# Kernel optimization log

Hardware: AMD Instinct MI355X
Metric: run time of the kernel (lower is better)

Reference implementation:

```python
import jax, jax.numpy as jnp
import numpy as np

SDIM, VDIM, HID, DEPTH = 128, 3, 64, 4
N, E = 50000, 800000
CUTOFF = 5.0


def setup_inputs() -> dict:
    key = jax.random.key(0)
    ks = jax.random.split(key, 16)
    s = jax.random.normal(ks[0], (N, SDIM), jnp.float32)
    v = jax.random.normal(ks[1], (N, 3, VDIM), jnp.float32)
    edge_index = jax.random.randint(ks[2], (2, E), 0, N, dtype=jnp.int32).astype(jnp.int64)
    d = jax.random.uniform(ks[3], (E,), jnp.float32) * CUTOFF
    r = jax.random.normal(ks[4], (E, 3), jnp.float32)
    r = r / jnp.linalg.norm(r, axis=-1, keepdims=True)
    batch = jnp.zeros((N,), jnp.int64)

    def w(k, shape):
        return jax.random.normal(k, shape, jnp.float32) / jnp.sqrt(jnp.float32(shape[-2]))

    return {
        's': s, 'v': v, 'edge_index': edge_index, 'd': d, 'r': r, 'batch': batch,
        'We1': w(ks[5], (DEPTH, 2 * SDIM + 1, HID)), 'be1': jnp.zeros((DEPTH, HID), jnp.float32),
        'We2': w(ks[6], (DEPTH, HID, HID)), 'be2': jnp.zeros((DEPTH, HID), jnp.float32),
        'Wn1': w(ks[7], (DEPTH, SDIM + HID, HID)), 'bn1': jnp.zeros((DEPTH, HID), jnp.float32),
        'Wn2': w(ks[8], (DEPTH, HID, SDIM)), 'bn2': jnp.zeros((DEPTH, SDIM), jnp.float32),
        'Wv': w(ks[9], (DEPTH, HID, 2 * VDIM)), 'bv': jnp.zeros((DEPTH, 2 * VDIM), jnp.float32),
    }


def _egcl(s, v, src, dst, d, r, C, deg, We1, be1, We2, be2, Wn1, bn1, Wn2, bn2, Wv, bv):
    n = s.shape[0]
    # edge message MLP on gathered endpoint features + distance
    x = jnp.concatenate([s[dst], s[src], d[:, None]], axis=-1)   # [E, 2*SDIM+1]
    h = jax.nn.silu(x @ We1 + be1)
    h = jax.nn.silu(h @ We2 + be2)
    h = h * C[:, None]                                            # cutoff envelope
    # scalar update
    agg_s = jax.ops.segment_sum(h, dst, num_segments=n)           # [N, HID]
    u = jax.nn.silu(jnp.concatenate([s, agg_s], axis=-1) @ Wn1 + bn1)
    s = s + (u @ Wn2 + bn2)
    # equivariant vector update: gated neighbor vectors + gated edge directions
    gates = h @ Wv + bv                                           # [E, 2*VDIM]
    g1, g2 = gates[:, :VDIM], gates[:, VDIM:]
    mv = v[src] * g1[:, None, :] + r[:, :, None] * g2[:, None, :] # [E, 3, VDIM]
    agg_v = jax.ops.segment_sum(mv, dst, num_segments=n) / deg[:, None, None]  # mean aggr
    v = v + agg_v
    return s, v


def reference(s, v, edge_index, d, r, batch, We1, be1, We2, be2, Wn1, bn1, Wn2, bn2, Wv, bv):
    src, dst = edge_index[0], edge_index[1]
    C = 0.5 * (jnp.cos(jnp.pi * d / CUTOFF) + 1.0) * (d < CUTOFF).astype(d.dtype)
    deg = jax.ops.segment_sum(jnp.ones_like(d), dst, num_segments=s.shape[0])
    deg = jnp.maximum(deg, 1.0)
    for i in range(DEPTH):
        s, v = _egcl(s, v, src, dst, d, r, C, deg,
                     We1[i], be1[i], We2[i], be2[i],
                     Wn1[i], bn1[i], Wn2[i], bn2[i], Wv[i], bv[i])
    return (s, v)
```

## Files before the change

### kernel.cpp

```cpp
#include <hip/hip_runtime.h>
#include <math.h>

#define SDIM 128
#define HID 64
#define DEPTH 4
#define CUTOFF_F 5.0f
#define CHUNK 4096

typedef __attribute__((ext_vector_type(8))) short bf16x8;
typedef __attribute__((ext_vector_type(4))) float f32x4;
typedef float4 __attribute__((aligned(4))) float4_u;

__device__ __forceinline__ float silu_f(float x) {
    float e = __expf(-x);
    return x * __builtin_amdgcn_rcpf(1.0f + e);
}

__device__ __forceinline__ unsigned short f2bf(float x) {
    __bf16 b = (__bf16)x;
    return __builtin_bit_cast(unsigned short, b);
}
__device__ __forceinline__ unsigned int f2bf2(float a, float b) {
    return (unsigned int)f2bf(a) | ((unsigned int)f2bf(b) << 16);
}
__device__ __forceinline__ float bf2f(unsigned short u) {
    return __uint_as_float(((unsigned int)u) << 16);
}

struct f8 { float v[8]; };
__device__ __forceinline__ f8 load8(const float* p) {
    f8 r;
    float4 a = *(const float4*)p;
    float4 b = *(const float4*)(p + 4);
    r.v[0]=a.x; r.v[1]=a.y; r.v[2]=a.z; r.v[3]=a.w;
    r.v[4]=b.x; r.v[5]=b.y; r.v[6]=b.z; r.v[7]=b.w;
    return r;
}
__device__ __forceinline__ bf16x8 pack8(const float* h) {
    bf16x8 o;
#pragma unroll
    for (int j = 0; j < 8; ++j) o[j] = (short)f2bf(h[j]);
    return o;
}
__device__ __forceinline__ void unpack8(bf16x8 b, float* o) {
#pragma unroll
    for (int j = 0; j < 8; ++j)
        o[j] = __uint_as_float(((unsigned int)(unsigned short)b[j]) << 16);
}

__global__ void detect_idx_kernel(const void* ei, int N, int* flag) {
    int lane = threadIdx.x;
    const long long* p64 = (const long long*)ei;
    long long v = p64[lane];
    bool ok = (v >= 0 && v < (long long)N);
    unsigned long long m = __ballot(ok);
    if (lane == 0) *flag = (m == ~0ull) ? 1 : 0;
}

__global__ void decode_idx_kernel(const void* ei, int E, int N, const int* flag,
                                  int* __restrict__ srcw, int* __restrict__ dstw,
                                  int* __restrict__ deg_i) {
    int i = blockIdx.x * blockDim.x + threadIdx.x;
    if (i >= 2 * E) return;
    int v;
    if (*flag) v = (int)((const long long*)ei)[i];
    else       v = ((const int*)ei)[i];
    v = min(max(v, 0), N - 1);
    if (i < E) {
        srcw[i] = v;
    } else {
        dstw[i - E] = v;
        atomicAdd(&deg_i[v], 1);
    }
}

__global__ __launch_bounds__(256) void scan1_kernel(const int* __restrict__ deg_i,
                                                    int* __restrict__ part, int N) {
    __shared__ int wsum[4];
    int b = blockIdx.x, t = threadIdx.x;
    int base = b * CHUNK;
    int sum = 0;
    for (int i = t; i < CHUNK; i += 256) {
        int idx = base + i;
        sum += (idx < N) ? deg_i[idx] : 0;
    }
#pragma unroll
    for (int off = 32; off; off >>= 1) sum += __shfl_down(sum, off, 64);
    if ((t & 63) == 0) wsum[t >> 6] = sum;
    __syncthreads();
    if (t == 0) part[b] = wsum[0] + wsum[1] + wsum[2] + wsum[3];
}

__global__ void scan2_kernel(int* __restrict__ part, int* __restrict__ row_start,
                             int B1, int N) {
    int t = threadIdx.x;
    int v = (t < B1) ? part[t] : 0;
    int incl = v;
#pragma unroll
    for (int off = 1; off < 64; off <<= 1) {
        int x = __shfl_up(incl, off, 64);
        if (t >= off) incl += x;
    }
    if (t < B1) part[t] = incl - v;
    if (t == 63) row_start[N] = incl;
}

__global__ __launch_bounds__(256) void scan3_kernel(const int* __restrict__ deg_i,
                                                    const int* __restrict__ part,
                                                    int* __restrict__ row_start, int N) {
    __shared__ int wsum[4];
    __shared__ int carry_s;
    int b = blockIdx.x, t = threadIdx.x;
    int lane = t & 63, w = t >> 6;
    if (t == 0) carry_s = part[b];
    __syncthreads();
    int base0 = b * CHUNK;
    for (int base = base0; base < base0 + CHUNK; base += 256) {
        int i = base + t;
        int v = (i < N) ? deg_i[i] : 0;
        int incl = v;
#pragma unroll
        for (int off = 1; off < 64; off <<= 1) {
            int x = __shfl_up(incl, off, 64);
            if (lane >= off) incl += x;
        }
        if (lane == 63) wsum[w] = incl;
        __syncthreads();
        int wpre = 0;
#pragma unroll
        for (int k = 0; k < 4; ++k) if (k < w) wpre += wsum[k];
        int total = wsum[0] + wsum[1] + wsum[2] + wsum[3];
        int carry = carry_s;
        if (i < N) row_start[i] = carry + wpre + incl - v;
        __syncthreads();
        if (t == 0) carry_s = carry + total;
        __syncthreads();
    }
}

__global__ void scatter_kernel(const int* __restrict__ srcw, const int* __restrict__ dstw,
                               const float* __restrict__ dvec, const float* __restrict__ rvec,
                               const int* __restrict__ row_start, int* __restrict__ cursor,
                               float* __restrict__ rec, int E) {
    int e = blockIdx.x * blockDim.x + threadIdx.x;
    if (e >= E) return;
    int dd = dstw[e];
    int ofs = atomicAdd(&cursor[dd], 1);
    int pos = row_start[dd] + ofs;
    float dv = dvec[e];
    float c = 0.5f * (cosf(3.14159265358979323846f * dv * (1.0f / CUTOFF_F)) + 1.0f);
    c = (dv < CUTOFF_F) ? c : 0.0f;
    float4 r0 = make_float4(__int_as_float(srcw[e]), __int_as_float(dd), dv, c);
    float4 r1 = make_float4(rvec[(size_t)e * 3 + 0], rvec[(size_t)e * 3 + 1],
                            rvec[(size_t)e * 3 + 2], 0.0f);
    *(float4*)(rec + (size_t)pos * 8)     = r0;
    *(float4*)(rec + (size_t)pos * 8 + 4) = r1;
}

__global__ __launch_bounds__(256) void wprep_kernel(
    const float* __restrict__ We1, const float* __restrict__ We2,
    const float* __restrict__ Wv,  const float* __restrict__ Wn1,
    const float* __restrict__ Wn2,
    unsigned short* __restrict__ We1t, unsigned short* __restrict__ We2t,
    unsigned short* __restrict__ Wvt,  unsigned short* __restrict__ Wn1t,
    unsigned short* __restrict__ Wn2t) {
    int l = blockIdx.x, t = threadIdx.x;
    const float* W2 = We2 + (size_t)l * HID * HID;
    unsigned short* T2 = We2t + (size_t)l * HID * HID;
    for (int idx = t; idx < HID * HID; idx += 256) {
        int n = idx >> 6, k = idx & 63;
        T2[n * 64 + k] = f2bf(W2[k * HID + n]);
    }
    const float* Wvl = Wv + (size_t)l * HID * 6;
    unsigned short* Tv = Wvt + (size_t)l * 16 * 64;
    for (int idx = t; idx < 16 * 64; idx += 256) {
        int n = idx >> 6, k = idx & 63;
        Tv[idx] = (n < 6) ? f2bf(Wvl[k * 6 + n]) : (unsigned short)0;
    }
    const float* W1 = We1 + (size_t)l * 257 * 64;
    unsigned short* T1 = We1t + (size_t)l * 128 * 128;
    for (int idx = t; idx < 128 * 128; idx += 256) {
        int n = idx >> 7, k = idx & 127;
        float w = (n < 64) ? W1[(size_t)k * 64 + n] : W1[(size_t)(k + 128) * 64 + (n - 64)];
        T1[n * 128 + k] = f2bf(w);
    }
    const float* Wn1l = Wn1 + (size_t)l * 192 * 64;
    unsigned short* Tn1 = Wn1t + (size_t)l * 64 * 192;
    for (int idx = t; idx < 64 * 192; idx += 256) {
        int n = idx / 192, k = idx - n * 192;
        Tn1[idx] = f2bf(Wn1l[(size_t)k * 64 + n]);
    }
    const float* Wn2l = Wn2 + (size_t)l * 64 * 128;
    unsigned short* Tn2 = Wn2t + (size_t)l * 128 * 64;
    for (int idx = t; idx < 128 * 64; idx += 256) {
        int n = idx >> 6, k = idx & 63;
        Tn2[idx] = f2bf(Wn2l[(size_t)k * 128 + n]);
    }
}

__global__ __launch_bounds__(64) void node_pre_kernel(
    const float* __restrict__ s, const unsigned short* __restrict__ We1t,
    const float* __restrict__ be1,
    unsigned short* __restrict__ Pa, unsigned short* __restrict__ Pb, int N)
{
    __shared__ unsigned short sa[16 * 136];
    int lane = threadIdx.x;
    int n0 = blockIdx.x * 16;
    for (int idx = lane; idx < 512; idx += 64) {
        int rl = idx >> 5, c4 = (idx & 31) << 2;
        int n = n0 + rl;
        float4 val = make_float4(0.f, 0.f, 0.f, 0.f);
        if (n < N) val = *(const float4*)(s + (size_t)n * SDIM + c4);
        *(uint2*)(sa + rl * 136 + c4) = make_uint2(f2bf2(val.x, val.y), f2bf2(val.z, val.w));
    }
    __builtin_amdgcn_wave_barrier();
    int lm = lane & 15, lq = lane >> 4;
    int nr = n0 + lm;
    bool rowok = (nr < N);

    bf16x8 af[4];
#pragma unroll
    for (int kc = 0; kc < 4; ++kc)
        af[kc] = *(const bf16x8*)(sa + lm * 136 + kc * 32 + lq * 8);

#pragma unroll
    for (int ct = 0; ct < 8; ++ct) {
        f32x4 acc = {0.f, 0.f, 0.f, 0.f};
#pragma unroll
        for (int kc = 0; kc < 4; ++kc) {
            bf16x8 b = *(const bf16x8*)(We1t + (size_t)(ct * 16 + lm) * 128 + kc * 32 + lq * 8);
            acc = __builtin_amdgcn_mfma_f32_16x16x32_bf16(b, af[kc], acc, 0, 0, 0);
        }
        if (rowok) {
            if (ct < 4) {
                float4 b4 = *(const float4*)(be1 + ct * 16 + lq * 4);
                *(uint2*)(Pa + (size_t)nr * HID + ct * 16 + lq * 4) =
                    make_uint2(f2bf2(acc[0] + b4.x, acc[1] + b4.y),
                               f2bf2(acc[2] + b4.z, acc[3] + b4.w));
            } else {
                *(uint2*)(Pb + (size_t)nr * HID + (ct - 4) * 16 + lq * 4) =
                    make_uint2(f2bf2(acc[0], acc[1]), f2bf2(acc[2], acc[3]));
            }
        }
    }
}

__global__ __launch_bounds__(256) void edge_kernel(
    const float* __restrict__ rec,
    const unsigned short* __restrict__ Pa, const unsigned short* __restrict__ Pb,
    const float* __restrict__ wd,
    const unsigned short* __restrict__ We2t, const float* __restrict__ be2,
    const unsigned short* __restrict__ Wvt, const float* __restrict__ bv,
    const float* __restrict__ v,
    float* __restrict__ agg_s, float* __restrict__ agg_v, int E)
{
    __shared__ unsigned short hb[64 * 72];
    __shared__ float  gl[64 * 8];
    __shared__ float  vb[64 * 12];
    __shared__ int    m_dst[64];
    __shared__ float4 m_r4[64];
    int t = threadIdx.x;
    int e0 = blockIdx.x * 64;
    int lane = t & 63, w = t >> 6;
    int lm = lane & 15, lq = lane >> 4;
    int m0 = w * 16, rm = m0 + lm;
    int ka = lq * 8, kb = 32 + lq * 8;

    int e  = e0 + rm;
    int ec = min(e, E - 1);
    float4 r0 = *(const float4*)(rec + (size_t)ec * 8);
    int srcr = __float_as_int(r0.x);
    int dstr = __float_as_int(r0.y);
    float dv = r0.z;
    float Cr = (e < E) ? r0.w : 0.0f;

    const unsigned short* pa = Pa + (size_t)dstr * HID;
    const unsigned short* pb = Pb + (size_t)srcr * HID;
    bf16x8 ba0 = *(const bf16x8*)(pa + ka);
    bf16x8 bb0 = *(const bf16x8*)(pb + ka);
    bf16x8 ba1 = *(const bf16x8*)(pa + kb);
    bf16x8 bb1 = *(const bf16x8*)(pb + kb);
    f8 xw = load8(wd + ka), yw = load8(wd + kb);

    if (lq == 0) {
        m_dst[rm] = dstr;
        m_r4[rm]  = *(const float4*)(rec + (size_t)ec * 8 + 4);
    }
    {
        const float* vr = v + (size_t)srcr * 9;
        if (lq < 2) {
            float4_u a = *(const float4_u*)(vr + lq * 4);
            *(float4*)(vb + rm * 12 + lq * 4) = make_float4(a.x, a.y, a.z, a.w);
        } else if (lq == 2) {
            vb[rm * 12 + 8] = vr[8];
        }
    }
    bf16x8 wv0 = *(const bf16x8*)(Wvt + (size_t)lm * 64 + ka);
    bf16x8 wv1 = *(const bf16x8*)(Wvt + (size_t)lm * 64 + kb);

    bf16x8 afr0, afr1;
    {
        float fa[8], fb[8], h1[8];
        unpack8(ba0, fa); unpack8(bb0, fb);
#pragma unroll
        for (int j = 0; j < 8; ++j) h1[j] = silu_f(fa[j] + fb[j] + dv * xw.v[j]);
        afr0 = pack8(h1);
        unpack8(ba1, fa); unpack8(bb1, fb);
#pragma unroll
        for (int j = 0; j < 8; ++j) h1[j] = silu_f(fa[j] + fb[j] + dv * yw.v[j]);
        afr1 = pack8(h1);
    }

#pragma unroll
    for (int t4 = 0; t4 < 4; ++t4) {
        bf16x8 a0 = *(const bf16x8*)(We2t + (size_t)(t4 * 16 + lm) * 64 + ka);
        bf16x8 a1 = *(const bf16x8*)(We2t + (size_t)(t4 * 16 + lm) * 64 + kb);
        f32x4 a = {0.f, 0.f, 0.f, 0.f};
        a = __builtin_amdgcn_mfma_f32_16x16x32_bf16(a0, afr0, a, 0, 0, 0);
        a = __builtin_amdgcn_mfma_f32_16x16x32_bf16(a1, afr1, a, 0, 0, 0);
        float4 b4 = *(const float4*)(be2 + t4 * 16 + lq * 4);
        unsigned int p0 = f2bf2(silu_f(a[0] + b4.x) * Cr, silu_f(a[1] + b4.y) * Cr);
        unsigned int p1 = f2bf2(silu_f(a[2] + b4.z) * Cr, silu_f(a[3] + b4.w) * Cr);
        *(uint2*)(hb + rm * 72 + t4 * 16 + lq * 4) = make_uint2(p0, p1);
    }
    __builtin_amdgcn_wave_barrier();

    {
        bf16x8 hb0 = *(const bf16x8*)(hb + rm * 72 + ka);
        bf16x8 hb1 = *(const bf16x8*)(hb + rm * 72 + kb);
        f32x4 ga = {0.f, 0.f, 0.f, 0.f};
        ga = __builtin_amdgcn_mfma_f32_16x16x32_bf16(wv0, hb0, ga, 0, 0, 0);
        ga = __builtin_amdgcn_mfma_f32_16x16x32_bf16(wv1, hb1, ga, 0, 0, 0);
        int er2 = m0 + lm;
        if (lq == 0) {
            float4_u bb = *(const float4_u*)bv;
            *(float4*)(gl + er2 * 8) =
                make_float4(ga[0] + bb.x, ga[1] + bb.y, ga[2] + bb.z, ga[3] + bb.w);
        } else if (lq == 1) {
            gl[er2 * 8 + 4] = ga[0] + bv[4];
            gl[er2 * 8 + 5] = ga[1] + bv[5];
        }
    }

    {
        int c = lane;
        float acc = 0.f;
        int cur = m_dst[m0];
#pragma unroll 4
        for (int r = m0; r < m0 + 16; ++r) {
            int dr = m_dst[r];
            if (dr != cur) {
                atomicAdd(&agg_s[(size_t)cur * HID + c], acc);
                acc = 0.f; cur = dr;
            }
            acc += bf2f(hb[r * 72 + c]);
        }
        atomicAdd(&agg_s[(size_t)cur * HID + c], acc);
    }
    __builtin_amdgcn_wave_barrier();

    if (lane < 36) {
        int seg = lane / 9;
        int c = lane - seg * 9;
        int i = c / 3, j = c - i * 3;
        int r0v = m0 + seg * 4;
        const float* mrf = (const float*)m_r4;
        float acc = 0.f;
        int cur = m_dst[r0v];
#pragma unroll
        for (int r = 0; r < 4; ++r) {
            int rr = r0v + r;
            int dr = m_dst[rr];
            if (dr != cur) {
                atomicAdd(&agg_v[(size_t)cur * 9 + c], acc);
                acc = 0.f; cur = dr;
            }
            if (e0 + rr < E) {
                acc += vb[rr * 12 + c] * gl[rr * 8 + j]
                     + mrf[rr * 4 + i] * gl[rr * 8 + 3 + j];
            }
        }
        atomicAdd(&agg_v[(size_t)cur * 9 + c], acc);
    }
}

__global__ __launch_bounds__(64) void node_fused_kernel(
    float* __restrict__ s, float* __restrict__ vout,
    float* __restrict__ agg_s, float* __restrict__ agg_v,
    const int* __restrict__ row_start,
    const unsigned short* __restrict__ Wn1t, const float* __restrict__ bn1,
    const unsigned short* __restrict__ Wn2t, const float* __restrict__ bn2,
    const unsigned short* __restrict__ We1tn, const float* __restrict__ be1n,
    unsigned short* __restrict__ Pa, unsigned short* __restrict__ Pb,
    int N, int do_pre)
{
    __shared__ unsigned short xa[16 * 200];
    __shared__ unsigned short ub[16 * 72];
    int lane = threadIdx.x;
    int n0 = blockIdx.x * 16;

    for (int idx = lane; idx < 144; idx += 64) {
        int rl = idx / 9, c = idx - rl * 9;
        int n2 = n0 + rl;
        if (n2 < N) {
            float av = agg_v[(size_t)n2 * 9 + c];
            agg_v[(size_t)n2 * 9 + c] = 0.f;
            float dg = fmaxf((float)(row_start[n2 + 1] - row_start[n2]), 1.0f);
            vout[(size_t)n2 * 9 + c] += av / dg;
        }
    }

    for (int idx = lane; idx < 512; idx += 64) {
        int rl = idx >> 5, c4 = (idx & 31) << 2;
        int n = n0 + rl;
        float4 val = make_float4(0.f, 0.f, 0.f, 0.f);
        if (n < N) val = *(const float4*)(s + (size_t)n * SDIM + c4);
        *(uint2*)(xa + rl * 200 + c4) = make_uint2(f2bf2(val.x, val.y), f2bf2(val.z, val.w));
    }
    for (int idx = lane; idx < 256; idx += 64) {
        int rl = idx >> 4, c4 = (idx & 15) << 2;
        int n = n0 + rl;
        float4 val = make_float4(0.f, 0.f, 0.f, 0.f);
        if (n < N) {
            float* ap = agg_s + (size_t)n * HID + c4;
            val = *(const float4*)ap;
            *(float4*)ap = make_float4(0.f, 0.f, 0.f, 0.f);
        }
        *(uint2*)(xa + rl * 200 + 128 + c4) = make_uint2(f2bf2(val.x, val.y), f2bf2(val.z, val.w));
    }
    __builtin_amdgcn_wave_barrier();

    int lm = lane & 15, lq = lane >> 4;
    int nr = n0 + lm;
    bool rowok = (nr < N);

    bf16x8 af[6];
#pragma unroll
    for (int kc = 0; kc < 6; ++kc)
        af[kc] = *(const bf16x8*)(xa + lm * 200 + kc * 32 + lq * 8);

#pragma unroll
    for (int ct = 0; ct < 4; ++ct) {
        f32x4 acc = {0.f, 0.f, 0.f, 0.f};
#pragma unroll
        for (int kc = 0; kc < 6; ++kc) {
            bf16x8 b = *(const bf16x8*)(Wn1t + (size_t)(ct * 16 + lm) * 192 + kc * 32 + lq * 8);
            acc = __builtin_amdgcn_mfma_f32_16x16x32_bf16(b, af[kc], acc, 0, 0, 0);
        }
        float4 b4 = *(const float4*)(bn1 + ct * 16 + lq * 4);
        unsigned int p0 = f2bf2(silu_f(acc[0] + b4.x), silu_f(acc[1] + b4.y));
        unsigned int p1 = f2bf2(silu_f(acc[2] + b4.z), silu_f(acc[3] + b4.w));
        *(uint2*)(ub + lm * 72 + ct * 16 + lq * 4) = make_uint2(p0, p1);
    }
    __builtin_amdgcn_wave_barrier();

    unsigned short* sa = xa;
    bf16x8 uf[2];
#pragma unroll
    for (int kc = 0; kc < 2; ++kc)
        uf[kc] = *(const bf16x8*)(ub + lm * 72 + kc * 32 + lq * 8);

    float4 sld[8];
#pragma unroll
    for (int ct = 0; ct < 8; ++ct)
        sld[ct] = rowok ? *(const float4*)(s + (size_t)nr * SDIM + ct * 16 + lq * 4)
                        : make_float4(0.f, 0.f, 0.f, 0.f);

#pragma unroll
    for (int ct = 0; ct < 8; ++ct) {
        f32x4 acc = {0.f, 0.f, 0.f, 0.f};
#pragma unroll
        for (int kc = 0; kc < 2; ++kc) {
            bf16x8 b = *(const bf16x8*)(Wn2t + (size_t)(ct * 16 + lm) * 64 + kc * 32 + lq * 8);
            acc = __builtin_amdgcn_mfma_f32_16x16x32_bf16(b, uf[kc], acc, 0, 0, 0);
        }
        float4 b4 = *(const float4*)(bn2 + ct * 16 + lq * 4);
        if (rowok) {
            float4 sv = make_float4(sld[ct].x + acc[0] + b4.x,
                                    sld[ct].y + acc[1] + b4.y,
                                    sld[ct].z + acc[2] + b4.z,
                                    sld[ct].w + acc[3] + b4.w);
            *(float4*)(s + (size_t)nr * SDIM + ct * 16 + lq * 4) = sv;
            *(uint2*)(sa + lm * 136 + ct * 16 + lq * 4) =
                make_uint2(f2bf2(sv.x, sv.y), f2bf2(sv.z, sv.w));
        } else {
            *(uint2*)(sa + lm * 136 + ct * 16 + lq * 4) = make_uint2(0u, 0u);
        }
    }
    __builtin_amdgcn_wave_barrier();

    if (do_pre) {
        bf16x8 pf[4];
#pragma unroll
        for (int kc = 0; kc < 4; ++kc)
            pf[kc] = *(const bf16x8*)(sa + lm * 136 + kc * 32 + lq * 8);

#pragma unroll
        for (int ct = 0; ct < 8; ++ct) {
            f32x4 acc = {0.f, 0.f, 0.f, 0.f};
#pragma unroll
            for (int kc = 0; kc < 4; ++kc) {
                bf16x8 b = *(const bf16x8*)(We1tn + (size_t)(ct * 16 + lm) * 128 + kc * 32 + lq * 8);
                acc = __builtin_amdgcn_mfma_f32_16x16x32_bf16(b, pf[kc], acc, 0, 0, 0);
            }
            if (rowok) {
                if (ct < 4) {
                    float4 b4 = *(const float4*)(be1n + ct * 16 + lq * 4);
                    *(uint2*)(Pa + (size_t)nr * HID + ct * 16 + lq * 4) =
                        make_uint2(f2bf2(acc[0] + b4.x, acc[1] + b4.y),
                                   f2bf2(acc[2] + b4.z, acc[3] + b4.w));
                } else {
                    *(uint2*)(Pb + (size_t)nr * HID + (ct - 4) * 16 + lq * 4) =
                        make_uint2(f2bf2(acc[0], acc[1]), f2bf2(acc[2], acc[3]));
                }
            }
        }
    }
}

extern "C" void kernel_launch(void* const* d_in, const int* in_sizes, int n_in,
                              void* d_out, int out_size, void* d_ws, size_t ws_size,
                              hipStream_t stream)
{
    const float* s_in  = (const float*)d_in[0];
    const float* v_in  = (const float*)d_in[1];
    const void*  ei    = d_in[2];
    const float* d_vec = (const float*)d_in[3];
    const float* r_vec = (const float*)d_in[4];
    const float* We1 = (const float*)d_in[6];
    const float* be1 = (const float*)d_in[7];
    const float* We2 = (const float*)d_in[8];
    const float* be2 = (const float*)d_in[9];
    const float* Wn1 = (const float*)d_in[10];
    const float* bn1 = (const float*)d_in[11];
    const float* Wn2 = (const float*)d_in[12];
    const float* bn2 = (const float*)d_in[13];
    const float* Wv  = (const float*)d_in[14];
    const float* bv  = (const float*)d_in[15];

    int N = in_sizes[0] / SDIM;
    int E = in_sizes[3];

    float* out_s = (float*)d_out;
    float* out_v = out_s + (size_t)N * SDIM;

    char* wp = (char*)d_ws;
    auto alloc = [&wp](size_t bytes) -> char* {
        char* p = wp;
        wp += (bytes + 31) & ~(size_t)31;
        return p;
    };
    float* rec       = (float*)alloc((size_t)E * 8 * 4);
    unsigned short* Pa = (unsigned short*)alloc((size_t)N * HID * 2);
    unsigned short* Pb = (unsigned short*)alloc((size_t)N * HID * 2);
    float* agg_s     = (float*)alloc((size_t)N * HID * 4);
    float* agg_v     = (float*)alloc((size_t)N * 9 * 4);
    int*   deg_i     = (int*)alloc((size_t)N * 4);
    int*   cursor    = (int*)alloc((size_t)N * 4);
    int*   row_start = (int*)alloc((size_t)(N + 1) * 4);
    int*   part      = (int*)alloc(64 * 4);
    int*   flag      = (int*)alloc(16);
    int*   srcw      = (int*)alloc((size_t)E * 4);
    int*   dstw      = (int*)alloc((size_t)E * 4);
    unsigned short* We2t = (unsigned short*)alloc((size_t)DEPTH * HID * HID * 2);
    unsigned short* Wvt  = (unsigned short*)alloc((size_t)DEPTH * 16 * 64 * 2);
    unsigned short* We1t = (unsigned short*)alloc((size_t)DEPTH * 128 * 128 * 2);
    unsigned short* Wn1t = (unsigned short*)alloc((size_t)DEPTH * 64 * 192 * 2);
    unsigned short* Wn2t = (unsigned short*)alloc((size_t)DEPTH * 128 * 64 * 2);

    hipMemcpyAsync(out_s, s_in, (size_t)N * SDIM * sizeof(float),
                   hipMemcpyDeviceToDevice, stream);
    hipMemcpyAsync(out_v, v_in, (size_t)N * 9 * sizeof(float),
                   hipMemcpyDeviceToDevice, stream);

    detect_idx_kernel<<<1, 64, 0, stream>>>(ei, N, flag);
    hipMemsetAsync(deg_i, 0, (size_t)N * 2 * sizeof(int), stream);
    hipMemsetAsync(agg_s, 0, (size_t)N * (HID + 9) * sizeof(float), stream);
    decode_idx_kernel<<<(2 * E + 255) / 256, 256, 0, stream>>>(ei, E, N, flag,
                                                               srcw, dstw, deg_i);
    int B1 = (N + CHUNK - 1) / CHUNK;
    scan1_kernel<<<B1, 256, 0, stream>>>(deg_i, part, N);
    scan2_kernel<<<1, 64, 0, stream>>>(part, row_start, B1, N);
    scan3_kernel<<<B1, 256, 0, stream>>>(deg_i, part, row_start, N);
    scatter_kernel<<<(E + 255) / 256, 256, 0, stream>>>(srcw, dstw, d_vec, r_vec,
                                                        row_start, cursor, rec, E);
    wprep_kernel<<<DEPTH, 256, 0, stream>>>(We1, We2, Wv, Wn1, Wn2,
                                            We1t, We2t, Wvt, Wn1t, Wn2t);

    int nb_n = (N + 15) / 16;
    int nb_e = (E + 63) / 64;
    node_pre_kernel<<<nb_n, 64, 0, stream>>>(out_s, We1t, be1, Pa, Pb, N);
    for (int l = 0; l < DEPTH; ++l) {
        int ln = (l + 1 < DEPTH) ? (l + 1) : 0;
        const float* We1_l = We1 + (size_t)l * 257 * 64;
        const float* be2_l = be2 + (size_t)l * 64;
        const float* bn1_l = bn1 + (size_t)l * 64;
        const float* bn2_l = bn2 + (size_t)l * 128;
        const float* bv_l  = bv  + (size_t)l * 6;
        const float* be1_n = be1 + (size_t)ln * 64;
        const unsigned short* We2t_l = We2t + (size_t)l * HID * HID;
        const unsigned short* Wvt_l  = Wvt  + (size_t)l * 16 * 64;
        const unsigned short* Wn1t_l = Wn1t + (size_t)l * 64 * 192;
        const unsigned short* Wn2t_l = Wn2t + (size_t)l * 128 * 64;
        const unsigned short* We1t_n = We1t + (size_t)ln * 128 * 128;

        edge_kernel<<<nb_e, 256, 0, stream>>>(rec, Pa, Pb,
                                              We1_l + 256 * 64,
                                              We2t_l, be2_l, Wvt_l, bv_l,
                                              out_v, agg_s, agg_v, E);
        node_fused_kernel<<<nb_n, 64, 0, stream>>>(out_s, out_v, agg_s, agg_v,
                                                   row_start,
                                                   Wn1t_l, bn1_l, Wn2t_l, bn2_l,
                                                   We1t_n, be1_n, Pa, Pb,
                                                   N, (l + 1 < DEPTH) ? 1 : 0);
    }
}
```

Before: 789.7 us.

## Replace atomic edge scatter with per-edge buffers and CSR gather in node kernel

Edges are already sorted by destination (CSR row_start). The edge kernel no longer does atomicAdd segment reductions. It writes each edge's scaled hidden message (bf16) and its 9-float vector message to per-edge buffers, and the node kernel reduces them deterministically by walking its CSR range. This removes atomic contention and the zeroing of the aggregation arrays. In exchange it adds roughly 128+36 bytes of write and read traffic per edge per layer, and the serial per-node loop in a 64-thread block may be latency-bound.

Result: slower. 973.6 us (+23.3%).

```diff
diff --git a/kernel.cpp b/kernel.cpp
--- a/kernel.cpp
+++ b/kernel.cpp
@@ -252,12 +252,11 @@
     const unsigned short* __restrict__ We2t, const float* __restrict__ be2,
     const unsigned short* __restrict__ Wvt, const float* __restrict__ bv,
     const float* __restrict__ v,
-    float* __restrict__ agg_s, float* __restrict__ agg_v, int E)
+    unsigned short* __restrict__ h_buf, float* __restrict__ mv_buf, int E)
 {
     __shared__ unsigned short hb[64 * 72];
     __shared__ float  gl[64 * 8];
     __shared__ float  vb[64 * 12];
-    __shared__ int    m_dst[64];
     __shared__ float4 m_r4[64];
     int t = threadIdx.x;
     int e0 = blockIdx.x * 64;
@@ -270,11 +269,10 @@
     int ec = min(e, E - 1);
     float4 r0 = *(const float4*)(rec + (size_t)ec * 8);
     int srcr = __float_as_int(r0.x);
-    int dstr = __float_as_int(r0.y);
     float dv = r0.z;
     float Cr = (e < E) ? r0.w : 0.0f;
 
-    const unsigned short* pa = Pa + (size_t)dstr * HID;
+    const unsigned short* pa = Pa + (size_t)__float_as_int(r0.y) * HID;
     const unsigned short* pb = Pb + (size_t)srcr * HID;
     bf16x8 ba0 = *(const bf16x8*)(pa + ka);
     bf16x8 bb0 = *(const bf16x8*)(pb + ka);
@@ -283,7 +281,6 @@
     f8 xw = load8(wd + ka), yw = load8(wd + kb);
 
     if (lq == 0) {
-        m_dst[rm] = dstr;
         m_r4[rm]  = *(const float4*)(rec + (size_t)ec * 8 + 4);
     }
     {
@@ -324,6 +321,15 @@
         *(uint2*)(hb + rm * 72 + t4 * 16 + lq * 4) = make_uint2(p0, p1);
     }
     __builtin_amdgcn_wave_barrier();
+
+#pragma unroll
+    for (int it = 0; it < 4; ++it) {
+        int r = m0 + it * 4 + (lane >> 4);
+        int c = (lane & 15) * 4;
+        int eg = e0 + r;
+        if (eg < E)
+            *(uint2*)(h_buf + (size_t)eg * 64 + c) = *(const uint2*)(hb + r * 72 + c);
+    }
 
     {
         bf16x8 hb0 = *(const bf16x8*)(hb + rm * 72 + ka);
@@ -341,52 +347,25 @@
             gl[er2 * 8 + 5] = ga[1] + bv[5];
         }
     }
-
-    {
-        int c = lane;
-        float acc = 0.f;
-        int cur = m_dst[m0];
-#pragma unroll 4
-        for (int r = m0; r < m0 + 16; ++r) {
-            int dr = m_dst[r];
-            if (dr != cur) {
-                atomicAdd(&agg_s[(size_t)cur * HID + c], acc);
-                acc = 0.f; cur = dr;
-            }
-            acc += bf2f(hb[r * 72 + c]);
-        }
-        atomicAdd(&agg_s[(size_t)cur * HID + c], acc);
-    }
     __builtin_amdgcn_wave_barrier();
 
-    if (lane < 36) {
-        int seg = lane / 9;
-        int c = lane - seg * 9;
+#pragma unroll
+    for (int k = lane; k < 144; k += 64) {
+        int rr = k / 9, c = k - rr * 9;
         int i = c / 3, j = c - i * 3;
-        int r0v = m0 + seg * 4;
-        const float* mrf = (const float*)m_r4;
-        float acc = 0.f;
-        int cur = m_dst[r0v];
-#pragma unroll
-        for (int r = 0; r < 4; ++r) {
-            int rr = r0v + r;
-            int dr = m_dst[rr];
-            if (dr != cur) {
-                atomicAdd(&agg_v[(size_t)cur * 9 + c], acc);
-                acc = 0.f; cur = dr;
-            }
-            if (e0 + rr < E) {
-                acc += vb[rr * 12 + c] * gl[rr * 8 + j]
-                     + mrf[rr * 4 + i] * gl[rr * 8 + 3 + j];
-            }
-        }
-        atomicAdd(&agg_v[(size_t)cur * 9 + c], acc);
+        int br = m0 + rr;
+        int eg = e0 + br;
+        if (eg < E) {
+            const float* mrf = (const float*)m_r4;
+            mv_buf[(size_t)eg * 9 + c] = vb[br * 12 + c] * gl[br * 8 + j]
+                                       + mrf[br * 4 + i] * gl[br * 8 + 3 + j];
+        }
     }
 }
 
 __global__ __launch_bounds__(64) void node_fused_kernel(
     float* __restrict__ s, float* __restrict__ vout,
-    float* __restrict__ agg_s, float* __restrict__ agg_v,
+    const unsigned short* __restrict__ h_buf, const float* __restrict__ mv_buf,
     const int* __restrict__ row_start,
     const unsigned short* __restrict__ Wn1t, const float* __restrict__ bn1,
     const unsigned short* __restrict__ Wn2t, const float* __restrict__ bn2,
@@ -396,19 +375,11 @@
 {
     __shared__ unsigned short xa[16 * 200];
     __shared__ unsigned short ub[16 * 72];
+    __shared__ int rs_s[17];
     int lane = threadIdx.x;
     int n0 = blockIdx.x * 16;
 
-    for (int idx = lane; idx < 144; idx += 64) {
-        int rl = idx / 9, c = idx - rl * 9;
-        int n2 = n0 + rl;
-        if (n2 < N) {
-            float av = agg_v[(size_t)n2 * 9 + c];
-            agg_v[(size_t)n2 * 9 + c] = 0.f;
-            float dg = fmaxf((float)(row_start[n2 + 1] - row_start[n2]), 1.0f);
-            vout[(size_t)n2 * 9 + c] += av / dg;
-        }
-    }
+    if (lane < 17) rs_s[lane] = row_start[min(n0 + lane, N)];
 
     for (int idx = lane; idx < 512; idx += 64) {
         int rl = idx >> 5, c4 = (idx & 31) << 2;
@@ -417,16 +388,33 @@
         if (n < N) val = *(const float4*)(s + (size_t)n * SDIM + c4);
         *(uint2*)(xa + rl * 200 + c4) = make_uint2(f2bf2(val.x, val.y), f2bf2(val.z, val.w));
     }
-    for (int idx = lane; idx < 256; idx += 64) {
-        int rl = idx >> 4, c4 = (idx & 15) << 2;
-        int n = n0 + rl;
-        float4 val = make_float4(0.f, 0.f, 0.f, 0.f);
-        if (n < N) {
-            float* ap = agg_s + (size_t)n * HID + c4;
-            val = *(const float4*)ap;
-            *(float4*)ap = make_float4(0.f, 0.f, 0.f, 0.f);
-        }
-        *(uint2*)(xa + rl * 200 + 128 + c4) = make_uint2(f2bf2(val.x, val.y), f2bf2(val.z, val.w));
+    __builtin_amdgcn_wave_barrier();
+
+    for (int rl = 0; rl < 16; ++rl) {
+        int eb = rs_s[rl], ee = rs_s[rl + 1];
+        float acc = 0.f;
+        int e2 = eb;
+        for (; e2 + 3 < ee; e2 += 4) {
+            float a0 = bf2f(h_buf[(size_t)e2 * 64 + lane]);
+            float a1 = bf2f(h_buf[(size_t)(e2 + 1) * 64 + lane]);
+            float a2 = bf2f(h_buf[(size_t)(e2 + 2) * 64 + lane]);
+            float a3 = bf2f(h_buf[(size_t)(e2 + 3) * 64 + lane]);
+            acc += (a0 + a1) + (a2 + a3);
+        }
+        for (; e2 < ee; ++e2) acc += bf2f(h_buf[(size_t)e2 * 64 + lane]);
+        xa[rl * 200 + 128 + lane] = f2bf(acc);
+    }
+
+    for (int k = lane; k < 144; k += 64) {
+        int rl = k / 9, c = k - rl * 9;
+        int eb = rs_s[rl], ee = rs_s[rl + 1];
+        float acc = 0.f;
+        for (int e2 = eb; e2 < ee; ++e2) acc += mv_buf[(size_t)e2 * 9 + c];
+        int n2 = n0 + rl;
+        if (n2 < N) {
+            float dg = fmaxf((float)(ee - eb), 1.0f);
+            vout[(size_t)n2 * 9 + c] += acc / dg;
+        }
     }
     __builtin_amdgcn_wave_barrier();
 
@@ -553,8 +541,8 @@
     float* rec       = (float*)alloc((size_t)E * 8 * 4);
     unsigned short* Pa = (unsigned short*)alloc((size_t)N * HID * 2);
     unsigned short* Pb = (unsigned short*)alloc((size_t)N * HID * 2);
-    float* agg_s     = (float*)alloc((size_t)N * HID * 4);
-    float* agg_v     = (float*)alloc((size_t)N * 9 * 4);
+    unsigned short* h_buf = (unsigned short*)alloc((size_t)E * HID * 2);
+    float* mv_buf    = (float*)alloc((size_t)E * 9 * 4);
     int*   deg_i     = (int*)alloc((size_t)N * 4);
     int*   cursor    = (int*)alloc((size_t)N * 4);
     int*   row_start = (int*)alloc((size_t)(N + 1) * 4);
@@ -575,7 +563,6 @@
 
     detect_idx_kernel<<<1, 64, 0, stream>>>(ei, N, flag);
     hipMemsetAsync(deg_i, 0, (size_t)N * 2 * sizeof(int), stream);
-    hipMemsetAsync(agg_s, 0, (size_t)N * (HID + 9) * sizeof(float), stream);
     decode_idx_kernel<<<(2 * E + 255) / 256, 256, 0, stream>>>(ei, E, N, flag,
                                                                srcw, dstw, deg_i);
     int B1 = (N + CHUNK - 1) / CHUNK;
@@ -607,8 +594,8 @@
         edge_kernel<<<nb_e, 256, 0, stream>>>(rec, Pa, Pb,
                                               We1_l + 256 * 64,
                                               We2t_l, be2_l, Wvt_l, bv_l,
-                                              out_v, agg_s, agg_v, E);
-        node_fused_kernel<<<nb_n, 64, 0, stream>>>(out_s, out_v, agg_s, agg_v,
+                                              out_v, h_buf, mv_buf, E);
+        node_fused_kernel<<<nb_n, 64, 0, stream>>>(out_s, out_v, h_buf, mv_buf,
                                                    row_start,
                                                    Wn1t_l, bn1_l, Wn2t_l, bn2_l,
                                                    We1t_n, be1_n, Pa, Pb,
```

## Process two 64-edge tiles per edge block with prefetched second-tile gathers

Applied to the files above, without the earlier changes.

Each edge_kernel block now handles 128 edges as two sequential 64-edge tiles. The gathers for the second tile (Pa/Pb rows, v rows, records) are issued early and overlap the first tile's MLP and atomic aggregation. Weight fragments and biases are reused across both tiles. In exchange the grid is half the size and register pressure rises from holding the prefetched fragments, which may reduce occupancy.

Result: slower. 824.4 us (+4.4%).

```diff
diff --git a/kernel.cpp b/kernel.cpp
--- a/kernel.cpp
+++ b/kernel.cpp
@@ -257,37 +257,45 @@
     __shared__ unsigned short hb[64 * 72];
     __shared__ float  gl[64 * 8];
     __shared__ float  vb[64 * 12];
-    __shared__ int    m_dst[64];
-    __shared__ float4 m_r4[64];
+    __shared__ int    m_dst[2][64];
+    __shared__ float4 m_r4[2][64];
     int t = threadIdx.x;
-    int e0 = blockIdx.x * 64;
+    int e0 = blockIdx.x * 128;
     int lane = t & 63, w = t >> 6;
     int lm = lane & 15, lq = lane >> 4;
     int m0 = w * 16, rm = m0 + lm;
     int ka = lq * 8, kb = 32 + lq * 8;
 
-    int e  = e0 + rm;
-    int ec = min(e, E - 1);
-    float4 r0 = *(const float4*)(rec + (size_t)ec * 8);
-    int srcr = __float_as_int(r0.x);
-    int dstr = __float_as_int(r0.y);
-    float dv = r0.z;
-    float Cr = (e < E) ? r0.w : 0.0f;
-
-    const unsigned short* pa = Pa + (size_t)dstr * HID;
-    const unsigned short* pb = Pb + (size_t)srcr * HID;
-    bf16x8 ba0 = *(const bf16x8*)(pa + ka);
-    bf16x8 bb0 = *(const bf16x8*)(pb + ka);
-    bf16x8 ba1 = *(const bf16x8*)(pa + kb);
-    bf16x8 bb1 = *(const bf16x8*)(pb + kb);
+    int eA = e0 + rm,      ecA = min(eA, E - 1);
+    int eB = e0 + 64 + rm, ecB = min(eB, E - 1);
+    float4 rA = *(const float4*)(rec + (size_t)ecA * 8);
+    float4 rB = *(const float4*)(rec + (size_t)ecB * 8);
+    int srcA = __float_as_int(rA.x), dstA = __float_as_int(rA.y);
+    float dvA = rA.z;
+    float CA = (eA < E) ? rA.w : 0.0f;
+    int srcB = __float_as_int(rB.x), dstB = __float_as_int(rB.y);
+    float dvB = rB.z;
+    float CB = (eB < E) ? rB.w : 0.0f;
+
+    const unsigned short* paA = Pa + (size_t)dstA * HID;
+    const unsigned short* pbA = Pb + (size_t)srcA * HID;
+    const unsigned short* pbB = Pb + (size_t)srcB * HID;
+    bf16x8 baA0 = *(const bf16x8*)(paA + ka);
+    bf16x8 bbA0 = *(const bf16x8*)(pbA + ka);
+    bf16x8 baA1 = *(const bf16x8*)(paA + kb);
+    bf16x8 bbA1 = *(const bf16x8*)(pbA + kb);
+    bf16x8 bbB0 = *(const bf16x8*)(pbB + ka);
+    bf16x8 bbB1 = *(const bf16x8*)(pbB + kb);
     f8 xw = load8(wd + ka), yw = load8(wd + kb);
 
     if (lq == 0) {
-        m_dst[rm] = dstr;
-        m_r4[rm]  = *(const float4*)(rec + (size_t)ec * 8 + 4);
+        m_dst[0][rm] = dstA;
+        m_r4[0][rm]  = *(const float4*)(rec + (size_t)ecA * 8 + 4);
+        m_dst[1][rm] = dstB;
+        m_r4[1][rm]  = *(const float4*)(rec + (size_t)ecB * 8 + 4);
     }
     {
-        const float* vr = v + (size_t)srcr * 9;
+        const float* vr = v + (size_t)srcA * 9;
         if (lq < 2) {
             float4_u a = *(const float4_u*)(vr + lq * 4);
             *(float4*)(vb + rm * 12 + lq * 4) = make_float4(a.x, a.y, a.z, a.w);
@@ -297,20 +305,21 @@
     }
     bf16x8 wv0 = *(const bf16x8*)(Wvt + (size_t)lm * 64 + ka);
     bf16x8 wv1 = *(const bf16x8*)(Wvt + (size_t)lm * 64 + kb);
+    float4_u bvv = *(const float4_u*)bv;
+    float bv4 = bv[4], bv5 = bv[5];
 
     bf16x8 afr0, afr1;
     {
         float fa[8], fb[8], h1[8];
-        unpack8(ba0, fa); unpack8(bb0, fb);
-#pragma unroll
-        for (int j = 0; j < 8; ++j) h1[j] = silu_f(fa[j] + fb[j] + dv * xw.v[j]);
+        unpack8(baA0, fa); unpack8(bbA0, fb);
+#pragma unroll
+        for (int j = 0; j < 8; ++j) h1[j] = silu_f(fa[j] + fb[j] + dvA * xw.v[j]);
         afr0 = pack8(h1);
-        unpack8(ba1, fa); unpack8(bb1, fb);
-#pragma unroll
-        for (int j = 0; j < 8; ++j) h1[j] = silu_f(fa[j] + fb[j] + dv * yw.v[j]);
+        unpack8(baA1, fa); unpack8(bbA1, fb);
+#pragma unroll
+        for (int j = 0; j < 8; ++j) h1[j] = silu_f(fa[j] + fb[j] + dvA * yw.v[j]);
         afr1 = pack8(h1);
     }
-
 #pragma unroll
     for (int t4 = 0; t4 < 4; ++t4) {
         bf16x8 a0 = *(const bf16x8*)(We2t + (size_t)(t4 * 16 + lm) * 64 + ka);
@@ -319,8 +328,8 @@
         a = __builtin_amdgcn_mfma_f32_16x16x32_bf16(a0, afr0, a, 0, 0, 0);
         a = __builtin_amdgcn_mfma_f32_16x16x32_bf16(a1, afr1, a, 0, 0, 0);
         float4 b4 = *(const float4*)(be2 + t4 * 16 + lq * 4);
-        unsigned int p0 = f2bf2(silu_f(a[0] + b4.x) * Cr, silu_f(a[1] + b4.y) * Cr);
-        unsigned int p1 = f2bf2(silu_f(a[2] + b4.z) * Cr, silu_f(a[3] + b4.w) * Cr);
+        unsigned int p0 = f2bf2(silu_f(a[0] + b4.x) * CA, silu_f(a[1] + b4.y) * CA);
+        unsigned int p1 = f2bf2(silu_f(a[2] + b4.z) * CA, silu_f(a[3] + b4.w) * CA);
         *(uint2*)(hb + rm * 72 + t4 * 16 + lq * 4) = make_uint2(p0, p1);
     }
     __builtin_amdgcn_wave_barrier();
@@ -333,22 +342,37 @@
         ga = __builtin_amdgcn_mfma_f32_16x16x32_bf16(wv1, hb1, ga, 0, 0, 0);
         int er2 = m0 + lm;
         if (lq == 0) {
-            float4_u bb = *(const float4_u*)bv;
             *(float4*)(gl + er2 * 8) =
-                make_float4(ga[0] + bb.x, ga[1] + bb.y, ga[2] + bb.z, ga[3] + bb.w);
+                make_float4(ga[0] + bvv.x, ga[1] + bvv.y, ga[2] + bvv.z, ga[3] + bvv.w);
         } else if (lq == 1) {
-            gl[er2 * 8 + 4] = ga[0] + bv[4];
-            gl[er2 * 8 + 5] = ga[1] + bv[5];
-        }
-    }
+            gl[er2 * 8 + 4] = ga[0] + bv4;
+            gl[er2 * 8 + 5] = ga[1] + bv5;
+        }
+    }
+
+    const unsigned short* paB = Pa + (size_t)dstB * HID;
+    bf16x8 baB0 = *(const bf16x8*)(paB + ka);
+    bf16x8 baB1 = *(const bf16x8*)(paB + kb);
+    float4 vB4 = make_float4(0.f, 0.f, 0.f, 0.f);
+    float vB8 = 0.f;
+    {
+        const float* vrB = v + (size_t)srcB * 9;
+        if (lq < 2) {
+            float4_u a = *(const float4_u*)(vrB + lq * 4);
+            vB4 = make_float4(a.x, a.y, a.z, a.w);
+        } else if (lq == 2) {
+            vB8 = vrB[8];
+        }
+    }
+    __builtin_amdgcn_wave_barrier();
 
     {
         int c = lane;
         float acc = 0.f;
-        int cur = m_dst[m0];
+        int cur = m_dst[0][m0];
 #pragma unroll 4
         for (int r = m0; r < m0 + 16; ++r) {
-            int dr = m_dst[r];
+            int dr = m_dst[0][r];
             if (dr != cur) {
                 atomicAdd(&agg_s[(size_t)cur * HID + c], acc);
                 acc = 0.f; cur = dr;
@@ -364,18 +388,107 @@
         int c = lane - seg * 9;
         int i = c / 3, j = c - i * 3;
         int r0v = m0 + seg * 4;
-        const float* mrf = (const float*)m_r4;
+        const float* mrf = (const float*)m_r4[0];
         float acc = 0.f;
-        int cur = m_dst[r0v];
+        int cur = m_dst[0][r0v];
 #pragma unroll
         for (int r = 0; r < 4; ++r) {
             int rr = r0v + r;
-            int dr = m_dst[rr];
+            int dr = m_dst[0][rr];
             if (dr != cur) {
                 atomicAdd(&agg_v[(size_t)cur * 9 + c], acc);
                 acc = 0.f; cur = dr;
             }
             if (e0 + rr < E) {
+                acc += vb[rr * 12 + c] * gl[rr * 8 + j]
+                     + mrf[rr * 4 + i] * gl[rr * 8 + 3 + j];
+            }
+        }
+        atomicAdd(&agg_v[(size_t)cur * 9 + c], acc);
+    }
+    __builtin_amdgcn_wave_barrier();
+
+    if (lq < 2) {
+        *(float4*)(vb + rm * 12 + lq * 4) = vB4;
+    } else if (lq == 2) {
+        vb[rm * 12 + 8] = vB8;
+    }
+    {
+        float fa[8], fb[8], h1[8];
+        unpack8(baB0, fa); unpack8(bbB0, fb);
+#pragma unroll
+        for (int j = 0; j < 8; ++j) h1[j] = silu_f(fa[j] + fb[j] + dvB * xw.v[j]);
+        afr0 = pack8(h1);
+        unpack8(baB1, fa); unpack8(bbB1, fb);
+#pragma unroll
+        for (int j = 0; j < 8; ++j) h1[j] = silu_f(fa[j] + fb[j] + dvB * yw.v[j]);
+        afr1 = pack8(h1);
+    }
+#pragma unroll
+    for (int t4 = 0; t4 < 4; ++t4) {
+        bf16x8 a0 = *(const bf16x8*)(We2t + (size_t)(t4 * 16 + lm) * 64 + ka);
+        bf16x8 a1 = *(const bf16x8*)(We2t + (size_t)(t4 * 16 + lm) * 64 + kb);
+        f32x4 a = {0.f, 0.f, 0.f, 0.f};
+        a = __builtin_amdgcn_mfma_f32_16x16x32_bf16(a0, afr0, a, 0, 0, 0);
+        a = __builtin_amdgcn_mfma_f32_16x16x32_bf16(a1, afr1, a, 0, 0, 0);
+        float4 b4 = *(const float4*)(be2 + t4 * 16 + lq * 4);
+        unsigned int p0 = f2bf2(silu_f(a[0] + b4.x) * CB, silu_f(a[1] + b4.y) * CB);
+        unsigned int p1 = f2bf2(silu_f(a[2] + b4.z) * CB, silu_f(a[3] + b4.w) * CB);
+        *(uint2*)(hb + rm * 72 + t4 * 16 + lq * 4) = make_uint2(p0, p1);
+    }
+    __builtin_amdgcn_wave_barrier();
+
+    {
+        bf16x8 hb0 = *(const bf16x8*)(hb + rm * 72 + ka);
+        bf16x8 hb1 = *(const bf16x8*)(hb + rm * 72 + kb);
+        f32x4 ga = {0.f, 0.f, 0.f, 0.f};
+        ga = __builtin_amdgcn_mfma_f32_16x16x32_bf16(wv0, hb0, ga, 0, 0, 0);
+        ga = __builtin_amdgcn_mfma_f32_16x16x32_bf16(wv1, hb1, ga, 0, 0, 0);
+        int er2 = m0 + lm;
+        if (lq == 0) {
+            *(float4*)(gl + er2 * 8) =
+                make_float4(ga[0] + bvv.x, ga[1] + bvv.y, ga[2] + bvv.z, ga[3] + bvv.w);
+        } else if (lq == 1) {
+            gl[er2 * 8 + 4] = ga[0] + bv4;
+            gl[er2 * 8 + 5] = ga[1] + bv5;
+        }
+    }
+    __builtin_amdgcn_wave_barrier();
+
+    {
+        int c = lane;
+        float acc = 0.f;
+        int cur = m_dst[1][m0];
+#pragma unroll 4
+        for (int r = m0; r < m0 + 16; ++r) {
+            int dr = m_dst[1][r];
+            if (dr != cur) {
+                atomicAdd(&agg_s[(size_t)cur * HID + c], acc);
+                acc = 0.f; cur = dr;
+            }
+            acc += bf2f(hb[r * 72 + c]);
+        }
+        atomicAdd(&agg_s[(size_t)cur * HID + c], acc);
+    }
+    __builtin_amdgcn_wave_barrier();
+
+    if (lane < 36) {
+        int seg = lane / 9;
+        int c = lane - seg * 9;
+        int i = c / 3, j = c - i * 3;
+        int r0v = m0 + seg * 4;
+        const float* mrf = (const float*)m_r4[1];
+        float acc = 0.f;
+        int cur = m_dst[1][r0v];
+#pragma unroll
+        for (int r = 0; r < 4; ++r) {
+            int rr = r0v + r;
+            int dr = m_dst[1][rr];
+            if (dr != cur) {
+                atomicAdd(&agg_v[(size_t)cur * 9 + c], acc);
+                acc = 0.f; cur = dr;
+            }
+            if (e0 + 64 + rr < E) {
                 acc += vb[rr * 12 + c] * gl[rr * 8 + j]
                      + mrf[rr * 4 + i] * gl[rr * 8 + 3 + j];
             }
@@ -588,7 +701,7 @@
                                             We1t, We2t, Wvt, Wn1t, Wn2t);
 
     int nb_n = (N + 15) / 16;
-    int nb_e = (E + 63) / 64;
+    int nb_e = (E + 127) / 128;
     node_pre_kernel<<<nb_n, 64, 0, stream>>>(out_s, We1t, be1, Pa, Pb, N);
     for (int l = 0; l < DEPTH; ++l) {
         int ln = (l + 1 < DEPTH) ? (l + 1) : 0;
```
